# Kernel tuning notes

Hardware: AMD Instinct MI355X
Metric: run time of the kernel (lower is better)

The kernel has to match this reference:

```python
import jax, jax.numpy as jnp
import numpy as np


def _ln(x, g, b, eps=1e-5):
    m = x.mean(-1, keepdims=True)
    v = ((x - m) ** 2).mean(-1, keepdims=True)
    return (x - m) * jax.lax.rsqrt(v + eps) * g + b


def setup_inputs() -> dict:
    key = jax.random.key(0)
    ks = jax.random.split(key, 12)
    B, S, I, H, E, P, O, EM = 32, 512, 64, 512, 8, 96, 64, 512
    D = S * I
    r = lambda k, shape, s=0.02: jax.random.normal(k, shape, jnp.float32) * s
    z = lambda *shape: jnp.zeros(shape, jnp.float32)
    o = lambda *shape: jnp.ones(shape, jnp.float32)
    return dict(
        x=jax.random.normal(ks[0], (B, S, I), jnp.float32),
        gW1=r(ks[1], (D, EM)), gb1=z(EM), gln1_g=o(EM), gln1_b=z(EM),
        gW2=r(ks[2], (EM, EM)), gb2=z(EM), gln2_g=o(EM), gln2_b=z(EM),
        gW3=r(ks[3], (EM, 128)), gb3=z(128),
        protos=jax.random.normal(ks[4], (E, 128), jnp.float32) * 0.01,
        temp=jnp.ones((), jnp.float32),
        eW1=r(ks[5], (E, I, H)), eb1=z(E, H),
        eW2=r(ks[6], (E, H, H)), eb2=z(E, H),
        fW1=r(ks[7], (H, H)), fb1=z(H), fln_g=o(H), fln_b=z(H),
        fW2=r(ks[8], (H, H)), fb2=z(H),
        ln_g=o(H), ln_b=z(H),
        pW1=r(ks[9], (H, H // 2)), pb1=z(H // 2), pln_g=o(H // 2), pln_b=z(H // 2),
        pW2=r(ks[10], (H // 2, P * O)), pb2=z(P * O),
        on_g=o(O), on_b=z(O),
    )


def reference(x, gW1, gb1, gln1_g, gln1_b, gW2, gb2, gln2_g, gln2_b, gW3, gb3,
              protos, temp, eW1, eb1, eW2, eb2,
              fW1, fb1, fln_g, fln_b, fW2, fb2, ln_g, ln_b,
              pW1, pb1, pln_g, pln_b, pW2, pb2, on_g, on_b):
    B, S, I = x.shape
    O = on_g.shape[0]
    P = pW2.shape[1] // O
    # 1) flow latent mapping (identity fallback path of the original code)
    x_flat = x.reshape(B, S * I)
    z_latent = x_flat
    # 2) gating encoder -> 128-d embedding (dropout = identity in eval)
    h = jax.nn.relu(_ln(z_latent @ gW1 + gb1, gln1_g, gln1_b))
    h = jax.nn.relu(_ln(h @ gW2 + gb2, gln2_g, gln2_b))
    emb = h @ gW3 + gb3  # [B, 128]
    # 3) routing: euclidean cdist to prototypes, temperature-scaled softmax
    d2 = jnp.sum((emb[:, None, :] - protos[None, :, :]) ** 2, axis=-1)
    dist = jnp.sqrt(jnp.maximum(d2, 1e-12))  # [B, E]
    t = jnp.clip(temp, 0.1, 5.0)
    w = jax.nn.softmax(-dist / t, axis=-1)  # [B, E]
    # 4) experts: per-expert FFN on raw input, all experts batched
    he = jax.nn.relu(jnp.einsum('bsi,eih->besh', x, eW1) + eb1[None, :, None, :])
    eo = jnp.einsum('besh,eho->beso', he, eW2) + eb2[None, :, None, :]  # [B,E,S,H]
    # 5) routing-weighted combine + fusion + prediction head
    fused = jnp.einsum('besh,be->bsh', eo, w)
    f = jax.nn.relu(_ln(fused @ fW1 + fb1, fln_g, fln_b)) @ fW2 + fb2
    f = _ln(f, ln_g, ln_b)
    last = f[:, -1, :]  # [B, H]
    p = jax.nn.relu(_ln(last @ pW1 + pb1, pln_g, pln_b)) @ pW2 + pb2
    p = p.reshape(B, P, O)
    return _ln(p, on_g, on_b)
```

## Files before the change

### kernel.cpp

```cpp
#include <hip/hip_runtime.h>
#include <math.h>

#define DIMK 32768

__device__ __forceinline__ void fma4(float4& a, float s, const float4 w) {
  a.x += s * w.x; a.y += s * w.y; a.z += s * w.z; a.w += s * w.w;
}

__device__ __forceinline__ float fsel(const float4& v, int kk) {
  return kk == 0 ? v.x : kk == 1 ? v.y : kk == 2 ? v.z : v.w;
}

__device__ __forceinline__ float block_sum(float v, float* red, int n) {
  int t = threadIdx.x;
  red[t] = v;
  __syncthreads();
  for (int s = n >> 1; s > 0; s >>= 1) {
    if (t < s) red[t] += red[t + s];
    __syncthreads();
  }
  float r = red[0];
  __syncthreads();
  return r;
}

__global__ __launch_bounds__(256) void gemm1(const float* __restrict__ x,
                                             const float* __restrict__ gW1,
                                             float* __restrict__ part) {
  const int mt = blockIdx.x, ks = blockIdx.y;
  const int m0 = mt * 256, k0 = ks * 256;
  const int t = threadIdx.x;
  __shared__ float As[32 * 256];
  __shared__ float Ws[32 * 256];

#pragma unroll
  for (int j = 0; j < 8; ++j) {
    int i = t + j * 256, b = i >> 6, q = i & 63;
    *(float4*)&As[b * 256 + q * 4] = *(const float4*)(x + (size_t)b * DIMK + k0 + q * 4);
  }
  const float* Wp = gW1 + (size_t)k0 * 512 + m0;
  float4 wreg[8];
#pragma unroll
  for (int j = 0; j < 8; ++j) {
    int i = t + j * 256, r = i >> 6, q = i & 63;
    wreg[j] = *(const float4*)(Wp + (size_t)r * 512 + q * 4);
  }

  const int mf4 = (t & 63) * 4;
  const int bg = t >> 6;
  float4 acc[8];
#pragma unroll
  for (int j = 0; j < 8; ++j) acc[j] = make_float4(0.f, 0.f, 0.f, 0.f);
  const float* a0 = &As[bg * 8 * 256];

  for (int s = 0; s < 8; ++s) {
    __syncthreads();
#pragma unroll
    for (int j = 0; j < 8; ++j) {
      int i = t + j * 256, r = i >> 6, q = i & 63;
      *(float4*)&Ws[r * 256 + q * 4] = wreg[j];
    }
    __syncthreads();
    if (s < 7) {
      const float* Wn = Wp + (size_t)(s + 1) * 32 * 512;
#pragma unroll
      for (int j = 0; j < 8; ++j) {
        int i = t + j * 256, r = i >> 6, q = i & 63;
        wreg[j] = *(const float4*)(Wn + (size_t)r * 512 + q * 4);
      }
    }
    const int sc = s * 32;
#pragma unroll
    for (int kq = 0; kq < 8; ++kq) {
      float4 av[8];
#pragma unroll
      for (int bb = 0; bb < 8; ++bb)
        av[bb] = *(const float4*)(a0 + bb * 256 + sc + kq * 4);
#pragma unroll
      for (int kk = 0; kk < 4; ++kk) {
        float4 wv = *(const float4*)&Ws[(kq * 4 + kk) * 256 + mf4];
        fma4(acc[0], fsel(av[0], kk), wv);
        fma4(acc[1], fsel(av[1], kk), wv);
        fma4(acc[2], fsel(av[2], kk), wv);
        fma4(acc[3], fsel(av[3], kk), wv);
        fma4(acc[4], fsel(av[4], kk), wv);
        fma4(acc[5], fsel(av[5], kk), wv);
        fma4(acc[6], fsel(av[6], kk), wv);
        fma4(acc[7], fsel(av[7], kk), wv);
      }
    }
  }

  float* op = part + ((size_t)ks * 32 + bg * 8) * 512 + m0 + mf4;
#pragma unroll
  for (int j = 0; j < 8; ++j) *(float4*)(op + (size_t)j * 512) = acc[j];
}

__global__ __launch_bounds__(512) void gred_ln(const float* __restrict__ part,
                                               const float* __restrict__ gb1,
                                               const float* __restrict__ g, const float* __restrict__ bt,
                                               float* __restrict__ h1) {
  const int b = blockIdx.x, t = threadIdx.x;
  __shared__ float red[512];
  float a = gb1[t];
  const float* pp0 = part + (size_t)b * 512 + t;
#pragma unroll 8
  for (int ks = 0; ks < 128; ++ks) a += pp0[(size_t)ks * 16384];
  float mean = block_sum(a, red, 512) * (1.f / 512.f);
  float d = a - mean;
  float var = block_sum(d * d, red, 512) * (1.f / 512.f);
  h1[b * 512 + t] = fmaxf(d * rsqrtf(var + 1e-5f) * g[t] + bt[t], 0.f);
}

template <int KC>
__global__ __launch_bounds__(256) void gemm_tile(const float* __restrict__ A,
                                                 const float* __restrict__ W,
                                                 float* __restrict__ outp,
                                                 int M, int aRow,
                                                 size_t aStrideE, size_t wStrideE) {
  const int mt = blockIdx.x, kq = blockIdx.y, e = blockIdx.z, NE = gridDim.z;
  const int m0 = mt * 64, k0 = kq * KC;
  const int t = threadIdx.x;
  __shared__ float Ws[KC * 64];
  __shared__ float As[32 * (KC + 4)];
  const float* Wp = W + (size_t)e * wStrideE + (size_t)k0 * M + m0;
  for (int i = t; i < KC * 16; i += 256) {
    int r = i >> 4, q = i & 15;
    *(float4*)&Ws[r * 64 + q * 4] = *(const float4*)(Wp + (size_t)r * M + q * 4);
  }
  const float* Ap = A + (size_t)e * aStrideE + k0;
  for (int i = t; i < 32 * (KC / 4); i += 256) {
    int b = i / (KC / 4), q = i % (KC / 4);
    *(float4*)&As[b * (KC + 4) + q * 4] = *(const float4*)(Ap + (size_t)b * aRow + q * 4);
  }
  __syncthreads();
  const int mf = t & 15, bg = t >> 4;
  const int b0 = bg * 2;
  float4 acc0 = make_float4(0.f, 0.f, 0.f, 0.f), acc1 = acc0;
  const float* a0 = &As[b0 * (KC + 4)];
  const float* a1 = &As[(b0 + 1) * (KC + 4)];
#pragma unroll 8
  for (int k = 0; k < KC; ++k) {
    float4 wv = *(const float4*)&Ws[k * 64 + mf * 4];
    fma4(acc0, a0[k], wv);
    fma4(acc1, a1[k], wv);
  }
  float* op = outp + ((size_t)(kq * NE + e) * 32 + b0) * M + m0 + mf * 4;
  *(float4*)op = acc0;
  *(float4*)(op + M) = acc1;
}

__global__ void red_ln(const float* __restrict__ zp, const float* __restrict__ bias,
                       const float* __restrict__ g, const float* __restrict__ bt,
                       float* __restrict__ outp, int M, int nq, int relu) {
  const int b = blockIdx.x, t = threadIdx.x;
  __shared__ float red[512];
  float a = bias[t];
#pragma unroll 4
  for (int kq = 0; kq < nq; ++kq) a += zp[((size_t)kq * 32 + b) * M + t];
  float fM = 1.f / (float)M;
  float mean = block_sum(a, red, M) * fM;
  float d = a - mean;
  float var = block_sum(d * d, red, M) * fM;
  float v = d * rsqrtf(var + 1e-5f) * g[t] + bt[t];
  outp[b * M + t] = relu ? fmaxf(v, 0.f) : v;
}

__global__ __launch_bounds__(128) void gate_k(const float* __restrict__ zp2,
                                              const float* __restrict__ gb3,
                                              const float* __restrict__ protos,
                                              const float* __restrict__ temp,
                                              float* __restrict__ wgt) {
  __shared__ float red[128];
  __shared__ float d2s[8];
  const int b = blockIdx.x, t = threadIdx.x;
  float a = gb3[t];
#pragma unroll 4
  for (int kq = 0; kq < 16; ++kq) a += zp2[((size_t)kq * 32 + b) * 128 + t];
  for (int e = 0; e < 8; ++e) {
    float dd = a - protos[e * 128 + t];
    float s = block_sum(dd * dd, red, 128);
    if (t == 0) d2s[e] = s;
  }
  __syncthreads();
  if (t == 0) {
    float tt = fminf(fmaxf(temp[0], 0.1f), 5.0f);
    float lg[8], mx = -1e30f;
#pragma unroll
    for (int e = 0; e < 8; ++e) {
      float dist = sqrtf(fmaxf(d2s[e], 1e-12f));
      lg[e] = -dist / tt;
      mx = fmaxf(mx, lg[e]);
    }
    float se = 0.f;
#pragma unroll
    for (int e = 0; e < 8; ++e) { lg[e] = expf(lg[e] - mx); se += lg[e]; }
#pragma unroll
    for (int e = 0; e < 8; ++e) wgt[b * 8 + e] = lg[e] / se;
  }
}

__global__ __launch_bounds__(256) void he_k(const float* __restrict__ x,
                                            const float* __restrict__ eW1,
                                            const float* __restrict__ eb1,
                                            float* __restrict__ he_all) {
  const int e = blockIdx.x, hs = blockIdx.y;
  const int t = threadIdx.x;
  __shared__ float xs[32 * 64];
  __shared__ float Ws[64 * 256];
  for (int i = t; i < 512; i += 256) {
    int b = i >> 4, q = i & 15;
    *(float4*)&xs[b * 64 + q * 4] = *(const float4*)(x + (size_t)b * DIMK + 32704 + q * 4);
  }
  const float* w1 = eW1 + (size_t)e * 64 * 512 + hs * 256;
  for (int i = t; i < 64 * 64; i += 256) {
    int k = i >> 6, q = i & 63;
    *(float4*)&Ws[k * 256 + q * 4] = *(const float4*)(w1 + (size_t)k * 512 + q * 4);
  }
  __syncthreads();
  float acc[32];
#pragma unroll
  for (int b = 0; b < 32; ++b) acc[b] = 0.f;
#pragma unroll 4
  for (int k = 0; k < 64; ++k) {
    float wk = Ws[k * 256 + t];
#pragma unroll
    for (int b = 0; b < 32; ++b) acc[b] += xs[b * 64 + k] * wk;
  }
  float bb = eb1[e * 512 + hs * 256 + t];
  for (int b = 0; b < 32; ++b)
    he_all[((size_t)e * 32 + b) * 512 + hs * 256 + t] = fmaxf(acc[b] + bb, 0.f);
}

__global__ __launch_bounds__(512) void ffuse(const float* __restrict__ epart,
                                             const float* __restrict__ eb2,
                                             const float* __restrict__ wgt,
                                             float* __restrict__ fused) {
  const int b = blockIdx.x, t = threadIdx.x;
  __shared__ float wl[8];
  if (t < 8) wl[t] = wgt[b * 8 + t];
  __syncthreads();
  float a = 0.f;
#pragma unroll
  for (int e = 0; e < 8; ++e) {
    float s = eb2[e * 512 + t];
#pragma unroll
    for (int kq = 0; kq < 8; ++kq)
      s += epart[(((size_t)kq * 8 + e) * 32 + b) * 512 + t];
    a += wl[e] * s;
  }
  fused[b * 512 + t] = a;
}

__global__ __launch_bounds__(256) void fin_red(const float* __restrict__ fpart,
                                               const float* __restrict__ pb2,
                                               const float* __restrict__ ong,
                                               const float* __restrict__ onb,
                                               float* __restrict__ outp) {
  const int t = threadIdx.x;
  const int lane = t & 63, w = t >> 6;
  const int r = blockIdx.x * 4 + w;
  const int b = r / 96, pi = r % 96;
  const int m = pi * 64 + lane;
  float a = pb2[m];
#pragma unroll
  for (int kq = 0; kq < 8; ++kq) a += fpart[((size_t)kq * 32 + b) * 6144 + m];
  float s = a;
  s += __shfl_xor(s, 1); s += __shfl_xor(s, 2); s += __shfl_xor(s, 4);
  s += __shfl_xor(s, 8); s += __shfl_xor(s, 16); s += __shfl_xor(s, 32);
  float mean = s * (1.f / 64.f);
  float d = a - mean;
  float q = d * d;
  q += __shfl_xor(q, 1); q += __shfl_xor(q, 2); q += __shfl_xor(q, 4);
  q += __shfl_xor(q, 8); q += __shfl_xor(q, 16); q += __shfl_xor(q, 32);
  float rr = rsqrtf(q * (1.f / 64.f) + 1e-5f);
  outp[((size_t)b * 96 + pi) * 64 + lane] = d * rr * ong[lane] + onb[lane];
}

extern "C" void kernel_launch(void* const* d_in, const int* in_sizes, int n_in,
                              void* d_out, int out_size, void* d_ws, size_t ws_size,
                              hipStream_t stream) {
  (void)in_sizes; (void)n_in; (void)out_size; (void)ws_size;
  const float* x      = (const float*)d_in[0];
  const float* gW1    = (const float*)d_in[1];
  const float* gb1    = (const float*)d_in[2];
  const float* gln1_g = (const float*)d_in[3];
  const float* gln1_b = (const float*)d_in[4];
  const float* gW2    = (const float*)d_in[5];
  const float* gb2    = (const float*)d_in[6];
  const float* gln2_g = (const float*)d_in[7];
  const float* gln2_b = (const float*)d_in[8];
  const float* gW3    = (const float*)d_in[9];
  const float* gb3    = (const float*)d_in[10];
  const float* protos = (const float*)d_in[11];
  const float* temp   = (const float*)d_in[12];
  const float* eW1    = (const float*)d_in[13];
  const float* eb1    = (const float*)d_in[14];
  const float* eW2    = (const float*)d_in[15];
  const float* eb2    = (const float*)d_in[16];
  const float* fW1    = (const float*)d_in[17];
  const float* fb1    = (const float*)d_in[18];
  const float* fln_g  = (const float*)d_in[19];
  const float* fln_b  = (const float*)d_in[20];
  const float* fW2    = (const float*)d_in[21];
  const float* fb2    = (const float*)d_in[22];
  const float* ln_g   = (const float*)d_in[23];
  const float* ln_b   = (const float*)d_in[24];
  const float* pW1    = (const float*)d_in[25];
  const float* pb1    = (const float*)d_in[26];
  const float* pln_g  = (const float*)d_in[27];
  const float* pln_b  = (const float*)d_in[28];
  const float* pW2    = (const float*)d_in[29];
  const float* pb2    = (const float*)d_in[30];
  const float* on_g   = (const float*)d_in[31];
  const float* on_b   = (const float*)d_in[32];
  float* out = (float*)d_out;

  float* ws     = (float*)d_ws;
  float* part   = ws;
  float* epart  = ws;
  float* he_all = ws + 1048576;
  float* fpart  = ws;
  float* h1     = ws + 2097152;
  float* h2     = h1 + 16384;
  float* zp     = h2 + 16384;
  float* zp2    = zp + 262144;
  float* wgt    = zp2 + 65536;
  float* fused  = wgt + 256;
  float* f1     = fused + 16384;
  float* lastv  = f1 + 16384;
  float* pp     = lastv + 16384;

  gemm1<<<dim3(2, 128), 256, 0, stream>>>(x, gW1, part);
  gred_ln<<<32, 512, 0, stream>>>(part, gb1, gln1_g, gln1_b, h1);
  gemm_tile<32><<<dim3(8, 16, 1), 256, 0, stream>>>(h1, gW2, zp, 512, 512, 0, 0);
  red_ln<<<32, 512, 0, stream>>>(zp, gb2, gln2_g, gln2_b, h2, 512, 16, 1);
  gemm_tile<32><<<dim3(2, 16, 1), 256, 0, stream>>>(h2, gW3, zp2, 128, 512, 0, 0);
  gate_k<<<32, 128, 0, stream>>>(zp2, gb3, protos, temp, wgt);

  he_k<<<dim3(8, 2), 256, 0, stream>>>(x, eW1, eb1, he_all);
  gemm_tile<64><<<dim3(8, 8, 8), 256, 0, stream>>>(he_all, eW2, epart, 512, 512,
                                                   (size_t)32 * 512, (size_t)512 * 512);
  ffuse<<<32, 512, 0, stream>>>(epart, eb2, wgt, fused);

  gemm_tile<32><<<dim3(8, 16, 1), 256, 0, stream>>>(fused, fW1, zp, 512, 512, 0, 0);
  red_ln<<<32, 512, 0, stream>>>(zp, fb1, fln_g, fln_b, f1, 512, 16, 1);
  gemm_tile<32><<<dim3(8, 16, 1), 256, 0, stream>>>(f1, fW2, zp, 512, 512, 0, 0);
  red_ln<<<32, 512, 0, stream>>>(zp, fb2, ln_g, ln_b, lastv, 512, 16, 0);
  gemm_tile<32><<<dim3(4, 16, 1), 256, 0, stream>>>(lastv, pW1, zp, 256, 512, 0, 0);
  red_ln<<<32, 256, 0, stream>>>(zp, pb1, pln_g, pln_b, pp, 256, 16, 1);

  gemm_tile<32><<<dim3(96, 8, 1), 256, 0, stream>>>(pp, pW2, fpart, 6144, 256, 0, 0);
  fin_red<<<768, 256, 0, stream>>>(fpart, pb2, on_g, on_b, out);
}
```

Baseline: 302.1 us.

## Use direct global-to-LDS loads in gemm1, two-stage reduction, larger K chunks

```diff
diff --git a/kernel.cpp b/kernel.cpp
--- a/kernel.cpp
+++ b/kernel.cpp
@@ -9,6 +9,12 @@
 
 __device__ __forceinline__ float fsel(const float4& v, int kk) {
   return kk == 0 ? v.x : kk == 1 ? v.y : kk == 2 ? v.z : v.w;
+}
+
+__device__ __forceinline__ void gld_lds16(const float* g, float* l) {
+  __builtin_amdgcn_global_load_lds(
+      (const __attribute__((address_space(1))) void*)g,
+      (__attribute__((address_space(3))) void*)l, 16, 0, 0);
 }
 
 __device__ __forceinline__ float block_sum(float v, float* red, int n) {
@@ -28,88 +34,73 @@
                                              const float* __restrict__ gW1,
                                              float* __restrict__ part) {
   const int mt = blockIdx.x, ks = blockIdx.y;
-  const int m0 = mt * 256, k0 = ks * 256;
+  const int m0 = mt * 128, k0 = ks * 256;
   const int t = threadIdx.x;
   __shared__ float As[32 * 256];
-  __shared__ float Ws[32 * 256];
+  __shared__ float Ws[2][32 * 128];
+
+  const float* Wp = gW1 + (size_t)k0 * 512 + m0;
 
 #pragma unroll
   for (int j = 0; j < 8; ++j) {
-    int i = t + j * 256, b = i >> 6, q = i & 63;
-    *(float4*)&As[b * 256 + q * 4] = *(const float4*)(x + (size_t)b * DIMK + k0 + q * 4);
-  }
-  const float* Wp = gW1 + (size_t)k0 * 512 + m0;
-  float4 wreg[8];
-#pragma unroll
-  for (int j = 0; j < 8; ++j) {
-    int i = t + j * 256, r = i >> 6, q = i & 63;
-    wreg[j] = *(const float4*)(Wp + (size_t)r * 512 + q * 4);
-  }
-
-  const int mf4 = (t & 63) * 4;
-  const int bg = t >> 6;
-  float4 acc[8];
-#pragma unroll
-  for (int j = 0; j < 8; ++j) acc[j] = make_float4(0.f, 0.f, 0.f, 0.f);
-  const float* a0 = &As[bg * 8 * 256];
+    int i = t + j * 256;
+    gld_lds16(x + (size_t)(i >> 6) * DIMK + k0 + (i & 63) * 4, &As[i * 4]);
+  }
+#pragma unroll
+  for (int j = 0; j < 4; ++j) {
+    int i = t + j * 256;
+    gld_lds16(Wp + (size_t)(i >> 5) * 512 + (i & 31) * 4, &Ws[0][i * 4]);
+  }
+
+  const int mf4 = (t & 31) * 4;
+  const int bg = t >> 5;
+  float4 acc[4];
+#pragma unroll
+  for (int j = 0; j < 4; ++j) acc[j] = make_float4(0.f, 0.f, 0.f, 0.f);
+  const float* a0 = &As[bg * 4 * 256];
 
   for (int s = 0; s < 8; ++s) {
-    __syncthreads();
-#pragma unroll
-    for (int j = 0; j < 8; ++j) {
-      int i = t + j * 256, r = i >> 6, q = i & 63;
-      *(float4*)&Ws[r * 256 + q * 4] = wreg[j];
-    }
     __syncthreads();
     if (s < 7) {
       const float* Wn = Wp + (size_t)(s + 1) * 32 * 512;
 #pragma unroll
-      for (int j = 0; j < 8; ++j) {
-        int i = t + j * 256, r = i >> 6, q = i & 63;
-        wreg[j] = *(const float4*)(Wn + (size_t)r * 512 + q * 4);
+      for (int j = 0; j < 4; ++j) {
+        int i = t + j * 256;
+        gld_lds16(Wn + (size_t)(i >> 5) * 512 + (i & 31) * 4, &Ws[(s + 1) & 1][i * 4]);
       }
     }
+    const float* Wc = Ws[s & 1];
     const int sc = s * 32;
 #pragma unroll
     for (int kq = 0; kq < 8; ++kq) {
-      float4 av[8];
-#pragma unroll
-      for (int bb = 0; bb < 8; ++bb)
-        av[bb] = *(const float4*)(a0 + bb * 256 + sc + kq * 4);
+      float4 av0 = *(const float4*)(a0 + sc + kq * 4);
+      float4 av1 = *(const float4*)(a0 + 256 + sc + kq * 4);
+      float4 av2 = *(const float4*)(a0 + 512 + sc + kq * 4);
+      float4 av3 = *(const float4*)(a0 + 768 + sc + kq * 4);
 #pragma unroll
       for (int kk = 0; kk < 4; ++kk) {
-        float4 wv = *(const float4*)&Ws[(kq * 4 + kk) * 256 + mf4];
-        fma4(acc[0], fsel(av[0], kk), wv);
-        fma4(acc[1], fsel(av[1], kk), wv);
-        fma4(acc[2], fsel(av[2], kk), wv);
-        fma4(acc[3], fsel(av[3], kk), wv);
-        fma4(acc[4], fsel(av[4], kk), wv);
-        fma4(acc[5], fsel(av[5], kk), wv);
-        fma4(acc[6], fsel(av[6], kk), wv);
-        fma4(acc[7], fsel(av[7], kk), wv);
+        float4 wv = *(const float4*)&Wc[(kq * 4 + kk) * 128 + mf4];
+        fma4(acc[0], fsel(av0, kk), wv);
+        fma4(acc[1], fsel(av1, kk), wv);
+        fma4(acc[2], fsel(av2, kk), wv);
+        fma4(acc[3], fsel(av3, kk), wv);
       }
     }
   }
 
-  float* op = part + ((size_t)ks * 32 + bg * 8) * 512 + m0 + mf4;
-#pragma unroll
-  for (int j = 0; j < 8; ++j) *(float4*)(op + (size_t)j * 512) = acc[j];
-}
-
-__global__ __launch_bounds__(512) void gred_ln(const float* __restrict__ part,
-                                               const float* __restrict__ gb1,
-                                               const float* __restrict__ g, const float* __restrict__ bt,
-                                               float* __restrict__ h1) {
-  const int b = blockIdx.x, t = threadIdx.x;
-  __shared__ float red[512];
-  float a = gb1[t];
-  const float* pp0 = part + (size_t)b * 512 + t;
-#pragma unroll 8
-  for (int ks = 0; ks < 128; ++ks) a += pp0[(size_t)ks * 16384];
-  float mean = block_sum(a, red, 512) * (1.f / 512.f);
-  float d = a - mean;
-  float var = block_sum(d * d, red, 512) * (1.f / 512.f);
-  h1[b * 512 + t] = fmaxf(d * rsqrtf(var + 1e-5f) * g[t] + bt[t], 0.f);
+  float* op = part + ((size_t)ks * 32 + bg * 4) * 512 + m0 + mf4;
+#pragma unroll
+  for (int j = 0; j < 4; ++j) *(float4*)(op + (size_t)j * 512) = acc[j];
+}
+
+__global__ __launch_bounds__(512) void part_red(const float* __restrict__ part,
+                                                float* __restrict__ pre) {
+  const int b = blockIdx.x, c = blockIdx.y, t = threadIdx.x;
+  float a = 0.f;
+  const float* p = part + ((size_t)c * 16 * 32 + b) * 512 + t;
+#pragma unroll
+  for (int i = 0; i < 16; ++i) a += p[(size_t)i * 16384];
+  pre[((size_t)c * 32 + b) * 512 + t] = a;
 }
 
 template <int KC>
@@ -175,8 +166,8 @@
   __shared__ float d2s[8];
   const int b = blockIdx.x, t = threadIdx.x;
   float a = gb3[t];
-#pragma unroll 4
-  for (int kq = 0; kq < 16; ++kq) a += zp2[((size_t)kq * 32 + b) * 128 + t];
+#pragma unroll
+  for (int kq = 0; kq < 8; ++kq) a += zp2[((size_t)kq * 32 + b) * 128 + t];
   for (int e = 0; e < 8; ++e) {
     float dd = a - protos[e * 128 + t];
     float s = block_sum(dd * dd, red, 128);
@@ -232,13 +223,13 @@
     he_all[((size_t)e * 32 + b) * 512 + hs * 256 + t] = fmaxf(acc[b] + bb, 0.f);
 }
 
-__global__ __launch_bounds__(512) void ffuse(const float* __restrict__ epart,
+__global__ __launch_bounds__(128) void ffuse(const float* __restrict__ epart,
                                              const float* __restrict__ eb2,
                                              const float* __restrict__ wgt,
                                              float* __restrict__ fused) {
-  const int b = blockIdx.x, t = threadIdx.x;
+  const int b = blockIdx.x, t = blockIdx.y * 128 + threadIdx.x;
   __shared__ float wl[8];
-  if (t < 8) wl[t] = wgt[b * 8 + t];
+  if (threadIdx.x < 8) wl[threadIdx.x] = wgt[b * 8 + threadIdx.x];
   __syncthreads();
   float a = 0.f;
 #pragma unroll
@@ -264,7 +255,7 @@
   const int m = pi * 64 + lane;
   float a = pb2[m];
 #pragma unroll
-  for (int kq = 0; kq < 8; ++kq) a += fpart[((size_t)kq * 32 + b) * 6144 + m];
+  for (int kq = 0; kq < 4; ++kq) a += fpart[((size_t)kq * 32 + b) * 6144 + m];
   float s = a;
   s += __shfl_xor(s, 1); s += __shfl_xor(s, 2); s += __shfl_xor(s, 4);
   s += __shfl_xor(s, 8); s += __shfl_xor(s, 16); s += __shfl_xor(s, 32);
@@ -331,25 +322,26 @@
   float* lastv  = f1 + 16384;
   float* pp     = lastv + 16384;
 
-  gemm1<<<dim3(2, 128), 256, 0, stream>>>(x, gW1, part);
-  gred_ln<<<32, 512, 0, stream>>>(part, gb1, gln1_g, gln1_b, h1);
-  gemm_tile<32><<<dim3(8, 16, 1), 256, 0, stream>>>(h1, gW2, zp, 512, 512, 0, 0);
-  red_ln<<<32, 512, 0, stream>>>(zp, gb2, gln2_g, gln2_b, h2, 512, 16, 1);
-  gemm_tile<32><<<dim3(2, 16, 1), 256, 0, stream>>>(h2, gW3, zp2, 128, 512, 0, 0);
+  gemm1<<<dim3(4, 128), 256, 0, stream>>>(x, gW1, part);
+  part_red<<<dim3(32, 8), 512, 0, stream>>>(part, zp);
+  red_ln<<<32, 512, 0, stream>>>(zp, gb1, gln1_g, gln1_b, h1, 512, 8, 1);
+  gemm_tile<64><<<dim3(8, 8, 1), 256, 0, stream>>>(h1, gW2, zp, 512, 512, 0, 0);
+  red_ln<<<32, 512, 0, stream>>>(zp, gb2, gln2_g, gln2_b, h2, 512, 8, 1);
+  gemm_tile<64><<<dim3(2, 8, 1), 256, 0, stream>>>(h2, gW3, zp2, 128, 512, 0, 0);
   gate_k<<<32, 128, 0, stream>>>(zp2, gb3, protos, temp, wgt);
 
   he_k<<<dim3(8, 2), 256, 0, stream>>>(x, eW1, eb1, he_all);
   gemm_tile<64><<<dim3(8, 8, 8), 256, 0, stream>>>(he_all, eW2, epart, 512, 512,
                                                    (size_t)32 * 512, (size_t)512 * 512);
-  ffuse<<<32, 512, 0, stream>>>(epart, eb2, wgt, fused);
-
-  gemm_tile<32><<<dim3(8, 16, 1), 256, 0, stream>>>(fused, fW1, zp, 512, 512, 0, 0);
-  red_ln<<<32, 512, 0, stream>>>(zp, fb1, fln_g, fln_b, f1, 512, 16, 1);
-  gemm_tile<32><<<dim3(8, 16, 1), 256, 0, stream>>>(f1, fW2, zp, 512, 512, 0, 0);
-  red_ln<<<32, 512, 0, stream>>>(zp, fb2, ln_g, ln_b, lastv, 512, 16, 0);
-  gemm_tile<32><<<dim3(4, 16, 1), 256, 0, stream>>>(lastv, pW1, zp, 256, 512, 0, 0);
-  red_ln<<<32, 256, 0, stream>>>(zp, pb1, pln_g, pln_b, pp, 256, 16, 1);
-
-  gemm_tile<32><<<dim3(96, 8, 1), 256, 0, stream>>>(pp, pW2, fpart, 6144, 256, 0, 0);
+  ffuse<<<dim3(32, 4), 128, 0, stream>>>(epart, eb2, wgt, fused);
+
+  gemm_tile<64><<<dim3(8, 8, 1), 256, 0, stream>>>(fused, fW1, zp, 512, 512, 0, 0);
+  red_ln<<<32, 512, 0, stream>>>(zp, fb1, fln_g, fln_b, f1, 512, 8, 1);
+  gemm_tile<64><<<dim3(8, 8, 1), 256, 0, stream>>>(f1, fW2, zp, 512, 512, 0, 0);
+  red_ln<<<32, 512, 0, stream>>>(zp, fb2, ln_g, ln_b, lastv, 512, 8, 0);
+  gemm_tile<64><<<dim3(4, 8, 1), 256, 0, stream>>>(lastv, pW1, zp, 256, 512, 0, 0);
+  red_ln<<<32, 256, 0, stream>>>(zp, pb1, pln_g, pln_b, pp, 256, 8, 1);
+
+  gemm_tile<64><<<dim3(96, 4, 1), 256, 0, stream>>>(pp, pW2, fpart, 6144, 256, 0, 0);
   fin_red<<<768, 256, 0, stream>>>(fpart, pb2, on_g, on_b, out);
 }
```

After: 276.8 us. 1.09x faster.
